# Kernel tuning notes

Measured on AMD Instinct MI355X. Metric: run time of the kernel, lower is better.

The kernel has to match this reference:

```python
import jax, jax.numpy as jnp
import numpy as np

C_CURV = 0.1            # curvature k
SC = float(np.sqrt(C_CURV))
EPS = 1e-7


def _mobius_add(x, y, c):
    x2 = jnp.sum(x * x, -1, keepdims=True)
    y2 = jnp.sum(y * y, -1, keepdims=True)
    xy = jnp.sum(x * y, -1, keepdims=True)
    num = (1 + 2 * c * xy + c * y2) * x + (1 - c * x2) * y
    den = 1 + 2 * c * xy + c * c * x2 * y2
    return num / jnp.maximum(den, 1e-12)


def _mobius_scalarmul(r, x, c):
    sc = jnp.sqrt(c)
    n = jnp.linalg.norm(x, axis=-1, keepdims=True)
    t = jnp.clip(sc * n, EPS, 1.0 - 1e-6)
    return jnp.tanh(r * jnp.arctanh(t)) * x / jnp.maximum(sc * n, EPS)


def setup_inputs() -> dict:
    key = jax.random.key(0)
    k0, k1, k2, k3, k4 = jax.random.split(key, 5)
    B, N, V, D, NC = 64, 1024, 50257, 128, 10
    token_ids = jax.random.randint(k0, (B, N), 0, V)
    mask = jax.random.randint(k1, (B, N), 0, 2).astype(bool)
    emb = (jax.random.normal(k2, (V, D), jnp.float32) * 0.02).at[0].set(0.0)  # pad_id=0 row zeroed
    Wo = jax.random.normal(k3, (D, D + 1), jnp.float32) / np.sqrt(D + 1)
    bo = jnp.zeros((D,), jnp.float32)
    Wf = jax.random.normal(k4, (NC, D), jnp.float32) / np.sqrt(D)
    bf = jnp.zeros((NC,), jnp.float32)
    return {"token_ids": token_ids, "mask": mask, "emb": emb, "Wo": Wo, "bo": bo, "Wf": Wf, "bf": bf}


def reference(token_ids, mask, emb, Wo, bo, Wf, bf):
    c, sc = C_CURV, SC
    D = emb.shape[1]
    # embedding lookup (tangent vectors at origin)
    v = emb[token_ids]                                            # (B,N,D)
    # Lorentz expmap0 -> hyperboloid points in D+1
    nv = jnp.maximum(jnp.linalg.norm(v, axis=-1, keepdims=True), EPS)
    x = jnp.concatenate([jnp.cosh(sc * nv) / sc,
                         jnp.sinh(sc * nv) * v / (sc * nv)], -1)  # (B,N,D+1)
    # single-head attention, scores = -<xi,xj>_L (Lorentz inner), masked softmax
    sgn = jnp.concatenate([-jnp.ones((1,)), jnp.ones((D,))]).astype(x.dtype)
    scores = -jnp.einsum('bid,bjd->bij', x * sgn, x) / np.sqrt(D + 1)
    scores = jnp.where(mask[:, None, :], scores, -1e9)
    w = jax.nn.softmax(scores, axis=-1)
    # riemannian value aggregation: Lorentz centroid (weighted sum renormalized to hyperboloid)
    mu = jnp.einsum('bij,bjd->bid', w, x)
    inner = jnp.einsum('bid,d,bid->bi', mu, sgn, mu)
    mu = mu / (sc * jnp.sqrt(jnp.maximum(-inner, EPS))[..., None])
    # output projection (D+1 -> D) then Poincare expmap0 so points lie in the ball
    u = jnp.einsum('bid,od->bio', mu, Wo) + bo                    # (B,N,D)
    nu = jnp.maximum(jnp.linalg.norm(u, axis=-1, keepdims=True), EPS)
    y = jnp.tanh(sc * nu) * u / (sc * nu)                         # (B,N,D) in ball
    # sequential masked Mobius pooling: left-fold mobius_add over valid tokens, then scalarmul 1/n
    def step(acc, xm):
        xi, mi = xm                                               # (B,D), (B,)
        new = _mobius_add(acc, xi, c)
        return jnp.where(mi[:, None], new, acc), None
    acc0 = jnp.zeros_like(y[:, 0, :])
    acc, _ = jax.lax.scan(step, acc0, (jnp.swapaxes(y, 0, 1), jnp.swapaxes(mask, 0, 1)))
    cnt = jnp.sum(mask, axis=1)
    r = (1.0 / jnp.maximum(cnt, 1))[:, None].astype(y.dtype)
    pooled = _mobius_scalarmul(r, acc, c)
    pooled = jnp.where((cnt > 0)[:, None], pooled, y[:, 0, :])    # empty rows fall back to first token
    # LorentzMLR head: logmap0 then linear
    npn = jnp.maximum(jnp.linalg.norm(pooled, axis=-1, keepdims=True), EPS)
    t = jnp.clip(sc * npn, EPS, 1.0 - 1e-6)
    vlog = jnp.arctanh(t) * pooled / (sc * npn)
    return vlog @ Wf.T + bf                                       # (B, num_classes)
```

## Files before the change

kernel.cpp:

```cpp
#include <hip/hip_runtime.h>
#include <math.h>

#define B_    64
#define N_    1024
#define D_    128
#define DP1   129
#define NC_   10
#define QB    128
#define KT    32
#define SCf   0.31622776601683794f
#define SCALE 0.08804509063256238f

typedef __bf16 bf16x8 __attribute__((ext_vector_type(8)));
typedef float  f32x16 __attribute__((ext_vector_type(16)));
typedef unsigned int  u32x4v __attribute__((ext_vector_type(4)));
typedef unsigned long long ull;

#define MFMA(a, b, c) __builtin_amdgcn_mfma_f32_32x32x16_bf16((a), (b), (c), 0, 0, 0)

static __device__ __forceinline__ unsigned pk_lo16(unsigned a, unsigned b) {
    return __builtin_amdgcn_perm(b, a, 0x05040100u);
}
static __device__ __forceinline__ unsigned pk_hi16(unsigned a, unsigned b) {
    return __builtin_amdgcn_perm(b, a, 0x07060302u);
}

static __device__ __forceinline__ float dpp_add_step(float f, int ctrl, int rmask) {
    if (ctrl == 0x111) { int t = __builtin_amdgcn_update_dpp(0, __builtin_bit_cast(int, f), 0x111, 0xf, 0xf, true); return f + __builtin_bit_cast(float, t); }
    if (ctrl == 0x112) { int t = __builtin_amdgcn_update_dpp(0, __builtin_bit_cast(int, f), 0x112, 0xf, 0xf, true); return f + __builtin_bit_cast(float, t); }
    if (ctrl == 0x114) { int t = __builtin_amdgcn_update_dpp(0, __builtin_bit_cast(int, f), 0x114, 0xf, 0xf, true); return f + __builtin_bit_cast(float, t); }
    if (ctrl == 0x118) { int t = __builtin_amdgcn_update_dpp(0, __builtin_bit_cast(int, f), 0x118, 0xf, 0xf, true); return f + __builtin_bit_cast(float, t); }
    if (ctrl == 0x142 && rmask == 0xa) { int t = __builtin_amdgcn_update_dpp(0, __builtin_bit_cast(int, f), 0x142, 0xa, 0xf, true); return f + __builtin_bit_cast(float, t); }
    { int t = __builtin_amdgcn_update_dpp(0, __builtin_bit_cast(int, f), 0x143, 0xc, 0xf, true); return f + __builtin_bit_cast(float, t); }
}

static __device__ __forceinline__ float wave_sum64(float f) {
    f = dpp_add_step(f, 0x111, 0xf);
    f = dpp_add_step(f, 0x112, 0xf);
    f = dpp_add_step(f, 0x114, 0xf);
    f = dpp_add_step(f, 0x118, 0xf);
    f = dpp_add_step(f, 0x142, 0xa);
    f = dpp_add_step(f, 0x143, 0xc);
    return __builtin_bit_cast(float, __builtin_amdgcn_readlane(__builtin_bit_cast(int, f), 63));
}

static __device__ __forceinline__ float half_sum32(float f, int half) {
    f = dpp_add_step(f, 0x111, 0xf);
    f = dpp_add_step(f, 0x112, 0xf);
    f = dpp_add_step(f, 0x114, 0xf);
    f = dpp_add_step(f, 0x118, 0xf);
    f = dpp_add_step(f, 0x142, 0xa);
    float s0 = __builtin_bit_cast(float, __builtin_amdgcn_readlane(__builtin_bit_cast(int, f), 31));
    float s1 = __builtin_bit_cast(float, __builtin_amdgcn_readlane(__builtin_bit_cast(int, f), 63));
    return half ? s1 : s0;
}

static __device__ __forceinline__ float readlane_f(float v, int lane) {
    return __builtin_bit_cast(float, __builtin_amdgcn_readlane(__builtin_bit_cast(int, v), lane));
}

static __device__ __forceinline__ bf16x8 ld_lds8(const __bf16* p) {
    union { bf16x8 v; ull q[2]; } u;
    u.q[0] = *(const ull*)(p);
    u.q[1] = *(const ull*)(p + 4);
    return u.v;
}

__global__ __launch_bounds__(256) void k_detect_mask(const int* __restrict__ mask_w,
                                                     int* __restrict__ flag) {
    __shared__ int bad;
    if (threadIdx.x == 0) bad = 0;
    __syncthreads();
    int local = 0;
    for (int i = threadIdx.x; i < 16384; i += 256) {
        int v = mask_w[i];
        if (v != 0 && v != 1) local = 1;
    }
    if (local) atomicOr(&bad, 1);
    __syncthreads();
    if (threadIdx.x == 0) *flag = bad;
}

static __device__ __forceinline__ int read_mask(const int* mw, int is_i8, int idx) {
    if (is_i8) return (int)((const unsigned char*)mw)[idx];
    return mw[idx];
}

__global__ __launch_bounds__(256) void k_prep_wo(const float* __restrict__ Wo,
                                                 __bf16* __restrict__ Woh,
                                                 __bf16* __restrict__ Wol) {
    int idx = blockIdx.x * 256 + threadIdx.x;
    if (idx >= 128 * 144) return;
    int o = idx / 144, d = idx - o * 144;
    float v = (d < DP1) ? Wo[o * DP1 + d] : 0.f;
    __bf16 h = (__bf16)v;
    Woh[idx] = h;
    Wol[idx] = (__bf16)(v - (float)h);
}

__global__ __launch_bounds__(256) void k_prep(const int* __restrict__ tok,
                                              const float* __restrict__ emb,
                                              __bf16* __restrict__ Xh, __bf16* __restrict__ Xl,
                                              float* __restrict__ X0g, float* __restrict__ X128g) {
    __shared__ float Xf[64][132];
    const int t = threadIdx.x, w = t >> 6, l = t & 63;
    const int base = blockIdx.x * 64;
    for (int it = 0; it < 16; ++it) {
        const int tk = w * 16 + it;
        const int id = tok[base + tk];
        const float2 v = ((const float2*)(emb + (size_t)id * D_))[l];
        float s = wave_sum64(v.x * v.x + v.y * v.y);
        float nv = fmaxf(sqrtf(s), 1e-7f);
        float a = SCf * nv;
        float a2 = a * a;
        float shc, ch;
        if (a < 0.5f) {
            shc = 1.f + a2 * (1.f/6.f) * (1.f + a2 * (1.f/20.f) * (1.f + a2 * (1.f/42.f)));
            ch  = 1.f + a2 * 0.5f * (1.f + a2 * (1.f/12.f) * (1.f + a2 * (1.f/30.f)));
        } else {
            float ea = __expf(a), ei = 1.f / ea;
            ch = 0.5f * (ea + ei);
            shc = 0.5f * (ea - ei) / a;
        }
        Xf[tk][1 + 2 * l] = v.x * shc;
        Xf[tk][2 + 2 * l] = v.y * shc;
        if (l == 0) Xf[tk][0] = ch / SCf;
    }
    __syncthreads();
    const int tk2 = t >> 2, dg = (t & 3) * 32;
    for (int i = 0; i < 32; i += 8) {
        bf16x8 hv, lv;
        #pragma unroll
        for (int j = 0; j < 8; ++j) {
            float f = Xf[tk2][dg + i + j];
            __bf16 h = (__bf16)f;
            hv[j] = h;
            lv[j] = (__bf16)(f - (float)h);
        }
        *(bf16x8*)(Xh + (size_t)(base + tk2) * D_ + dg + i) = hv;
        *(bf16x8*)(Xl + (size_t)(base + tk2) * D_ + dg + i) = lv;
    }
    if (t < 64) {
        X0g[base + t]   = Xf[t][0];
        X128g[base + t] = Xf[t][D_];
    }
}

__global__ __launch_bounds__(256, 2) void k_attn(
        const __bf16* __restrict__ Xh, const __bf16* __restrict__ Xl,
        const float* __restrict__ X0g, const float* __restrict__ X128g,
        const int* __restrict__ mask, const int* __restrict__ mflag,
        const __bf16* __restrict__ Woh, const __bf16* __restrict__ Wol,
        const float* __restrict__ bo,
        float* __restrict__ Y, float* __restrict__ Y2) {
    extern __shared__ char smem[];
    unsigned* KBI = (unsigned*)smem;
    unsigned* Pbi = (unsigned*)(smem + 33792);
    __shared__ float K0s[2][KT];
    __shared__ float K128s[2][KT];
    __shared__ int   Ms[2][KT];

    const int b    = blockIdx.x;
    const int qb   = blockIdx.y * QB;
    const int t    = threadIdx.x;
    const int w    = t >> 6;
    const int l    = t & 63;
    const int l31  = l & 31;
    const int half = l >> 5;
    const int is8  = *mflag;

    const size_t qrow = (size_t)(b * N_ + qb + w * 32 + l31);
    bf16x8 qfh[8], qfl[8];
    #pragma unroll
    for (int ks = 0; ks < 8; ++ks) {
        qfh[ks] = *(const bf16x8*)(Xh + qrow * D_ + ks * 16 + half * 8);
        qfl[ks] = *(const bf16x8*)(Xl + qrow * D_ + ks * 16 + half * 8);
    }
    float q0[16], q128[16];
    #pragma unroll
    for (int r = 0; r < 16; ++r) {
        const int qr = (r & 3) + 8 * (r >> 2) + 4 * half;
        q0[r]   = X0g[b * N_ + qb + w * 32 + qr];
        q128[r] = X128g[b * N_ + qb + w * 32 + qr];
    }

    const int skey = t >> 3, sck = t & 7;
    bf16x8 svh0, svh1, svl0, svl1;
    float  sK0 = 0.f, sK128 = 0.f;
    int    sM = 0;
    auto ldg_tile = [&](int kt) {
        const size_t kr = (size_t)(b * N_ + kt * KT + skey);
        svh0 = *(const bf16x8*)(Xh + kr * D_ + sck * 16);
        svh1 = *(const bf16x8*)(Xh + kr * D_ + sck * 16 + 8);
        svl0 = *(const bf16x8*)(Xl + kr * D_ + sck * 16);
        svl1 = *(const bf16x8*)(Xl + kr * D_ + sck * 16 + 8);
        if (t < KT) {
            sK0   = X0g[b * N_ + kt * KT + t];
            sK128 = X128g[b * N_ + kt * KT + t];
            sM    = read_mask(mask, is8, b * N_ + kt * KT + t);
        }
    };
    auto st_tile = [&](int buf) {
        unsigned* KI = KBI + buf * 4224;
        union { bf16x8 v; unsigned d[4]; } H0, H1, L0, L1;
        H0.v = svh0; H1.v = svh1; L0.v = svl0; L1.v = svl1;
        u32x4v o0 = { pk_lo16(H0.d[0], L0.d[0]), pk_hi16(H0.d[0], L0.d[0]),
                      pk_lo16(H0.d[1], L0.d[1]), pk_hi16(H0.d[1], L0.d[1]) };
        u32x4v o1 = { pk_lo16(H0.d[2], L0.d[2]), pk_hi16(H0.d[2], L0.d[2]),
                      pk_lo16(H0.d[3], L0.d[3]), pk_hi16(H0.d[3], L0.d[3]) };
        u32x4v o2 = { pk_lo16(H1.d[0], L1.d[0]), pk_hi16(H1.d[0], L1.d[0]),
                      pk_lo16(H1.d[1], L1.d[1]), pk_hi16(H1.d[1], L1.d[1]) };
        u32x4v o3 = { pk_lo16(H1.d[2], L1.d[2]), pk_hi16(H1.d[2], L1.d[2]),
                      pk_lo16(H1.d[3], L1.d[3]), pk_hi16(H1.d[3], L1.d[3]) };
        u32x4v* dst = (u32x4v*)(KI + skey * 132 + sck * 16);
        dst[0] = o0; dst[1] = o1; dst[2] = o2; dst[3] = o3;
        if (t < KT) { K0s[buf][t] = sK0; K128s[buf][t] = sK128; Ms[buf][t] = sM; }
    };

    f32x16 accM[4] = {};
    float  mu128p[16] = {};

    ldg_tile(0);
    st_tile(0);

    for (int kt = 0; kt < N_ / KT; ++kt) {
        __syncthreads();
        const int cur = kt & 1;
        const int ktn = (kt < 31) ? kt + 1 : 31;
        ldg_tile(ktn);

        const unsigned* KI = KBI + cur * 4224;

        f32x16 accS = {};
        #pragma unroll
        for (int ks = 0; ks < 8; ++ks) {
            const unsigned* p = KI + l31 * 132 + ks * 16 + half * 8;
            u32x4v ua = *(const u32x4v*)(p);
            u32x4v ub = *(const u32x4v*)(p + 4);
            union { bf16x8 v; unsigned d[4]; } BH, BL;
            BH.d[0] = pk_lo16(ua[0], ua[1]); BL.d[0] = pk_hi16(ua[0], ua[1]);
            BH.d[1] = pk_lo16(ua[2], ua[3]); BL.d[1] = pk_hi16(ua[2], ua[3]);
            BH.d[2] = pk_lo16(ub[0], ub[1]); BL.d[2] = pk_hi16(ub[0], ub[1]);
            BH.d[3] = pk_lo16(ub[2], ub[3]); BL.d[3] = pk_hi16(ub[2], ub[3]);
            accS = MFMA(qfh[ks], BH.v, accS);
            accS = MFMA(qfh[ks], BL.v, accS);
            accS = MFMA(qfl[ks], BH.v, accS);
        }
        const float k0v = K0s[cur][l31], k128v = K128s[cur][l31];
        const int   mv  = Ms[cur][l31];
        #pragma unroll
        for (int r = 0; r < 16; ++r) {
            float sc = (2.f * q0[r] * k0v - accS[r] - q128[r] * k128v) * SCALE;
            float e  = mv ? __expf(sc) : 0.f;
            mu128p[r] += e * k128v;
            __bf16 eh = (__bf16)e;
            __bf16 el = (__bf16)(e - (float)eh);
            unsigned pw = (unsigned)__builtin_bit_cast(unsigned short, eh)
                        | ((unsigned)__builtin_bit_cast(unsigned short, el) << 16);
            const int qr = (r & 3) + 8 * (r >> 2) + 4 * half;
            Pbi[w * 1152 + qr * 36 + l31] = pw;
        }

        #pragma unroll
        for (int ks = 0; ks < 2; ++ks) {
            const unsigned* pp = Pbi + w * 1152 + l31 * 36 + ks * 16 + half * 8;
            u32x4v pa = *(const u32x4v*)(pp);
            u32x4v pb = *(const u32x4v*)(pp + 4);
            union { bf16x8 v; unsigned d[4]; } AH, AL;
            AH.d[0] = pk_lo16(pa[0], pa[1]); AL.d[0] = pk_hi16(pa[0], pa[1]);
            AH.d[1] = pk_lo16(pa[2], pa[3]); AL.d[1] = pk_hi16(pa[2], pa[3]);
            AH.d[2] = pk_lo16(pb[0], pb[1]); AL.d[2] = pk_hi16(pb[0], pb[1]);
            AH.d[3] = pk_lo16(pb[2], pb[3]); AL.d[3] = pk_hi16(pb[2], pb[3]);
            #pragma unroll
            for (int nt = 0; nt < 4; ++nt) {
                const unsigned* kb = KI + (ks * 16 + half * 8) * 132 + nt * 32 + l31;
                unsigned u[8];
                #pragma unroll
                for (int j = 0; j < 8; ++j) u[j] = kb[j * 132];
                union { bf16x8 v; unsigned d[4]; } BH, BL;
                BH.d[0] = pk_lo16(u[0], u[1]); BL.d[0] = pk_hi16(u[0], u[1]);
                BH.d[1] = pk_lo16(u[2], u[3]); BL.d[1] = pk_hi16(u[2], u[3]);
                BH.d[2] = pk_lo16(u[4], u[5]); BL.d[2] = pk_hi16(u[4], u[5]);
                BH.d[3] = pk_lo16(u[6], u[7]); BL.d[3] = pk_hi16(u[6], u[7]);
                accM[nt] = MFMA(AH.v, BH.v, accM[nt]);
                accM[nt] = MFMA(AH.v, BL.v, accM[nt]);
                accM[nt] = MFMA(AL.v, BH.v, accM[nt]);
            }
        }

        st_tile(cur ^ 1);
    }

    #pragma unroll
    for (int r = 0; r < 16; ++r) mu128p[r] = half_sum32(mu128p[r], half);
    float rno[16];
    #pragma unroll
    for (int r = 0; r < 16; ++r) {
        float p = 0.f;
        #pragma unroll
        for (int nt = 0; nt < 4; ++nt) p += accM[nt][r] * accM[nt][r];
        if (l31 == 0) p -= 2.f * accM[0][r] * accM[0][r];
        p = half_sum32(p, half);
        float negI = -(p + mu128p[r] * mu128p[r]);
        negI = fmaxf(negI, 1e-7f);
        rno[r] = 1.f / (SCf * sqrtf(negI));
    }
    #pragma unroll
    for (int nt = 0; nt < 4; ++nt)
        #pragma unroll
        for (int r = 0; r < 16; ++r) accM[nt][r] *= rno[r];
    #pragma unroll
    for (int r = 0; r < 16; ++r) mu128p[r] *= rno[r];

    __syncthreads();
    __bf16* MuA = (__bf16*)smem + w * (32 * 148);
    #pragma unroll
    for (int r = 0; r < 16; ++r) {
        const int qr = (r & 3) + 8 * (r >> 2) + 4 * half;
        #pragma unroll
        for (int nt = 0; nt < 4; ++nt)
            MuA[qr * 148 + nt * 32 + l31] = (__bf16)accM[nt][r];
        if (l31 == 0) MuA[qr * 148 + 128] = (__bf16)mu128p[r];
        if (l31 >= 1 && l31 <= 15) MuA[qr * 148 + 128 + l31] = (__bf16)0.f;
    }
    bf16x8 Ah[9];
    #pragma unroll
    for (int ks = 0; ks < 9; ++ks) Ah[ks] = ld_lds8(MuA + l31 * 148 + ks * 16 + half * 8);
    #pragma unroll
    for (int r = 0; r < 16; ++r) {
        const int qr = (r & 3) + 8 * (r >> 2) + 4 * half;
        #pragma unroll
        for (int nt = 0; nt < 4; ++nt) {
            float m = accM[nt][r];
            MuA[qr * 148 + nt * 32 + l31] = (__bf16)(m - (float)(__bf16)m);
        }
        if (l31 == 0) {
            float m = mu128p[r];
            MuA[qr * 148 + 128] = (__bf16)(m - (float)(__bf16)m);
        }
    }
    bf16x8 Al[9];
    #pragma unroll
    for (int ks = 0; ks < 9; ++ks) Al[ks] = ld_lds8(MuA + l31 * 148 + ks * 16 + half * 8);

    f32x16 accU[4] = {};
    #pragma unroll
    for (int ks = 0; ks < 9; ++ks) {
        #pragma unroll
        for (int nt = 0; nt < 4; ++nt) {
            bf16x8 bh = *(const bf16x8*)(Woh + (size_t)(nt * 32 + l31) * 144 + ks * 16 + half * 8);
            bf16x8 bl = *(const bf16x8*)(Wol + (size_t)(nt * 32 + l31) * 144 + ks * 16 + half * 8);
            accU[nt] = MFMA(Ah[ks], bh, accU[nt]);
            accU[nt] = MFMA(Ah[ks], bl, accU[nt]);
            accU[nt] = MFMA(Al[ks], bh, accU[nt]);
        }
    }

    float bov[4];
    #pragma unroll
    for (int nt = 0; nt < 4; ++nt) bov[nt] = bo[nt * 32 + l31];
    #pragma unroll
    for (int r = 0; r < 16; ++r) {
        float p = 0.f;
        #pragma unroll
        for (int nt = 0; nt < 4; ++nt) {
            float uv = accU[nt][r] + bov[nt];
            accU[nt][r] = uv;
            p += uv * uv;
        }
        float nn = half_sum32(p, half);
        float nu = fmaxf(sqrtf(nn), 1e-7f);
        float aa = SCf * nu;
        float cf = tanhf(aa) / aa;
        const int qr = (r & 3) + 8 * (r >> 2) + 4 * half;
        const size_t row = (size_t)(b * N_ + qb + w * 32 + qr);
        #pragma unroll
        for (int nt = 0; nt < 4; ++nt)
            Y[row * D_ + nt * 32 + l31] = accU[nt][r] * cf;
        if (l31 == 0) Y2[row] = nn * cf * cf;
    }
}

__global__ __launch_bounds__(256) void k_gram(const float* __restrict__ Y,
                                              float* __restrict__ G) {
    const int c = blockIdx.x, b = blockIdx.y;
    const int t = threadIdx.x, w = t >> 6, l = t & 63;
    const int l31 = l & 31, half = l >> 5;
    const int rt = w >> 1, ct = w & 1;
    const size_t base = (size_t)(b * N_ + c * 64);
    const float* Ar = Y + (base + rt * 32 + l31) * D_;
    const float* Br = Y + (base + ct * 32 + l31) * D_;
    f32x16 acc = {};
    #pragma unroll
    for (int ks = 0; ks < 8; ++ks) {
        const int c0 = ks * 16 + half * 8;
        float4 a0 = *(const float4*)(Ar + c0);
        float4 a1 = *(const float4*)(Ar + c0 + 4);
        float4 b0 = *(const float4*)(Br + c0);
        float4 b1 = *(const float4*)(Br + c0 + 4);
        float av[8] = {a0.x, a0.y, a0.z, a0.w, a1.x, a1.y, a1.z, a1.w};
        float bv[8] = {b0.x, b0.y, b0.z, b0.w, b1.x, b1.y, b1.z, b1.w};
        bf16x8 ah, al, bh, bl;
        #pragma unroll
        for (int j = 0; j < 8; ++j) {
            __bf16 h = (__bf16)av[j]; ah[j] = h; al[j] = (__bf16)(av[j] - (float)h);
            __bf16 g = (__bf16)bv[j]; bh[j] = g; bl[j] = (__bf16)(bv[j] - (float)g);
        }
        acc = MFMA(ah, bh, acc);
        acc = MFMA(ah, bl, acc);
        acc = MFMA(al, bh, acc);
    }
    float* Gb = G + ((size_t)(b * 16 + c) << 12);
    #pragma unroll
    for (int r = 0; r < 16; ++r) {
        const int row = rt * 32 + (r & 3) + 8 * (r >> 2) + 4 * half;
        Gb[row * 64 + ct * 32 + l31] = acc[r];
    }
}

__global__ __launch_bounds__(64, 1) void k_pool(const float* __restrict__ Y,
                                                const float* __restrict__ Y2,
                                                const float* __restrict__ G,
                                                const int* __restrict__ mask,
                                                const int* __restrict__ mflag,
                                                const float* __restrict__ Wf,
                                                const float* __restrict__ bf_,
                                                float* __restrict__ out) {
    __shared__ float  prt[64][65];
    __shared__ double vb[D_];
    const int b = blockIdx.x, l = threadIdx.x;
    const int is8 = *mflag;

    int cl = 0;
    for (int i = l; i < N_; i += 64) cl += read_mask(mask, is8, b * N_ + i);
    const int cntT = (int)(wave_sum64((float)cl) + 0.5f);

    const float2* __restrict__ Yp = (const float2*)(Y + (size_t)b * N_ * D_) + l;
    const float*  __restrict__ Gp = G + ((size_t)b << 16) + l;
    const float*  __restrict__ Pp = Y2 + b * N_;

    float  GA[64], GB[64];
    float  py2A, py2B;
    int    msA, msB;
    float2 yring[2][16];

    #pragma unroll
    for (int i = 0; i < 64; ++i) GA[i] = Gp[i * 64];
    py2A = Pp[l];
    msA  = read_mask(mask, is8, b * N_ + l);
    #pragma unroll
    for (int k = 0; k < 16; ++k) yring[0][k] = Yp[(size_t)k * 64];

    float U0 = 0.f, U1 = 0.f, g = 0.f, Dh = 1.f, P = 0.f;

    auto chunk = [&](int c, float (&Gc)[64], float (&Gn)[64],
                     float py2c, float& py2n, int msc, int& msn) {
        const int cn = (c < 15) ? c + 1 : 15;
        #pragma unroll
        for (int i = 0; i < 64; ++i) Gn[i] = Gp[cn * 4096 + i * 64];
        py2n = Pp[cn * 64 + l];
        msn  = read_mask(mask, is8, b * N_ + cn * 64 + l);

        #pragma unroll
        for (int q = 0; q < 4; ++q) {
            #pragma unroll
            for (int k = 0; k < 16; ++k) {
                int gs = c * 64 + (q + 1) * 16 + k;
                if (gs > N_ - 1) gs = N_ - 1;
                yring[(q + 1) & 1][k] = Yp[(size_t)gs * 64];
            }
            #pragma unroll
            for (int k = 0; k < 16; ++k) {
                const int ir = q * 16 + k;
                const float2 yv  = yring[q & 1][k];
                const float  Gv  = Gc[ir];
                const float  py2 = readlane_f(py2c, ir);
                const bool   m   = (__builtin_amdgcn_readlane(msc, ir) != 0);
                const float Dsq   = Dh * Dh;
                const float Bh    = fmaf(-0.1f, P, Dsq);
                const float Donep = Dh * fmaf(0.1f, py2, 1.f);
                const float tP    = (0.01f * py2) * P;
                const float puy  = readlane_f(g, ir);
                const float Ahat = fmaf(0.2f, puy, Donep);
                float dh = fmaf(Dh, fmaf(0.2f, puy, Dh), tP);
                dh = fmaxf(dh, 1e-12f * Dsq);
                const float Draw = m ? dh : Dh;
                const float Am   = m ? Ahat : 1.f;
                const float Bm   = m ? Bh   : 0.f;
                const float Pn   = fmaf(Am, fmaf(Am, P, (2.f * Bm) * puy), (Bm * Bm) * py2);
                if ((k & 3) == 3) {
                    const int e = ilogbf(Draw);
                    const float Aef = ldexpf(Am, -e);
                    const float Bef = ldexpf(Bm, -e);
                    Dh = ldexpf(Draw, -e);
                    P  = ldexpf(Pn, -2 * e);
                    g  = fmaf(Aef, g, Bef * Gv);
                    U0 = fmaf(Aef, U0, Bef * yv.x);
                    U1 = fmaf(Aef, U1, Bef * yv.y);
                } else {
                    Dh = Draw;
                    P  = Pn;
                    g  = fmaf(Am, g, Bm * Gv);
                    U0 = fmaf(Am, U0, Bm * yv.x);
                    U1 = fmaf(Am, U1, Bm * yv.y);
                }
            }
        }
        if (c < 15) {
            const int nb = (c + 1) * 64;
            #pragma unroll
            for (int k0 = 0; k0 < 64; k0 += 16) {
                float2 tmp[16];
                #pragma unroll
                for (int k = 0; k < 16; ++k) tmp[k] = Yp[(size_t)(nb + k0 + k) * 64];
                #pragma unroll
                for (int k = 0; k < 16; ++k)
                    prt[k0 + k][l] = fmaf(U0, tmp[k].x, U1 * tmp[k].y);
            }
            float s0 = 0.f, s1 = 0.f, s2 = 0.f, s3 = 0.f;
            #pragma unroll
            for (int p = 0; p < 64; p += 4) {
                s0 += prt[l][p];     s1 += prt[l][p + 1];
                s2 += prt[l][p + 2]; s3 += prt[l][p + 3];
            }
            g = (s0 + s1) + (s2 + s3);
        }
    };

    for (int cc = 0; cc < 8; ++cc) {
        chunk(2 * cc,     GA, GB, py2A, py2B, msA, msB);
        chunk(2 * cc + 1, GB, GA, py2B, py2A, msB, msA);
    }

    const double SCd = 0.31622776601683794;
    const double sD = 1.0 / (double)Dh;
    double a0 = sD * (double)U0, a1 = sD * (double)U1;
    double n2 = fmax((double)P * (sD * sD), 0.0);
    double n = sqrt(n2);
    double tt = SCd * n;
    tt = fmin(fmax(tt, 1e-7), 1.0 - 1e-6);
    int cm = cntT > 0 ? cntT : 1;
    float rf = (float)(1.0 / (double)cm);
    double r = (double)rf;
    double dv = fmax(SCd * n, 1e-7);
    double f = tanh(r * atanh(tt)) / dv;
    double p0 = a0 * f, p1 = a1 * f;
    double q2;
    if (cntT == 0) {
        float2 y0v = *(const float2*)(Y + (size_t)(b * N_) * D_ + 2 * l);
        p0 = y0v.x; p1 = y0v.y;
        q2 = (double)Y2[b * N_];
    } else {
        q2 = f * f * n2;
    }
    double npn = fmax(sqrt(q2), 1e-7);
    double t2 = fmin(fmax(SCd * npn, 1e-7), 1.0 - 1e-6);
    double f2 = atanh(t2) / (SCd * npn);
    vb[2 * l]     = p0 * f2;
    vb[2 * l + 1] = p1 * f2;
    __syncthreads();

    if (l < NC_) {
        double o = (double)bf_[l];
        for (int d = 0; d < D_; ++d) o += vb[d] * (double)Wf[l * D_ + d];
        out[b * NC_ + l] = (float)o;
    }
}

extern "C" void kernel_launch(void* const* d_in, const int* in_sizes, int n_in,
                              void* d_out, int out_size, void* d_ws, size_t ws_size,
                              hipStream_t stream) {
    const int*   tok  = (const int*)d_in[0];
    const int*   mask = (const int*)d_in[1];
    const float* emb  = (const float*)d_in[2];
    const float* Wo   = (const float*)d_in[3];
    const float* bo   = (const float*)d_in[4];
    const float* Wf   = (const float*)d_in[5];
    const float* bf_  = (const float*)d_in[6];
    float* out = (float*)d_out;

    char* wsb = (char*)d_ws;
    __bf16* Xh   = (__bf16*)wsb;
    __bf16* Xl   = (__bf16*)(wsb + 16777216);
    float*  X0g  = (float*)(wsb + 33554432);
    float*  X128g= (float*)(wsb + 33816576);
    __bf16* Woh  = (__bf16*)(wsb + 34078720);
    __bf16* Wol  = (__bf16*)(wsb + 34115584);
    float*  Y    = (float*)(wsb + 34152448);
    float*  Y2   = (float*)(wsb + 67706880);
    int*    flag = (int*)(wsb + 67969024);
    float*  Gram = (float*)wsb;

    k_detect_mask<<<dim3(1), dim3(256), 0, stream>>>(mask, flag);
    k_prep_wo<<<dim3(72), dim3(256), 0, stream>>>(Wo, Woh, Wol);
    k_prep<<<dim3(B_ * N_ / 64), dim3(256), 0, stream>>>(tok, emb, Xh, Xl, X0g, X128g);
    k_attn<<<dim3(B_, N_ / QB), dim3(256), 52224, stream>>>(Xh, Xl, X0g, X128g, mask, flag,
                                                            Woh, Wol, bo, Y, Y2);
    k_gram<<<dim3(16, B_), dim3(256), 0, stream>>>(Y, Gram);
    k_pool<<<dim3(B_), dim3(64), 0, stream>>>(Y, Y2, Gram, mask, flag, Wf, bf_, out);
}
```

Before: 392.7 us.

## Fuse prep kernels into one launch and compute Gram blocks inside attention

Merges mask detection, Wo split and embedding prep into a single kernel launch, using extra blocks for the small side tasks. When the workspace is large enough, the attention kernel stages its output Y tile in shared memory and computes the 64x64 Gram blocks directly with split-bf16 MFMAs. This removes the separate k_gram pass that re-reads Y from global memory and saves launch overhead. In exchange it adds extra syncs and LDS reuse at the tail of attention, and requires an extra 16MB workspace region, falling back to the old path otherwise.

New measurement: 388.0 us. Within noise of the previous version (-1.2%).

```diff
diff --git a/kernel.cpp b/kernel.cpp
--- a/kernel.cpp
+++ b/kernel.cpp
@@ -66,44 +66,46 @@
     return u.v;
 }
 
-__global__ __launch_bounds__(256) void k_detect_mask(const int* __restrict__ mask_w,
-                                                     int* __restrict__ flag) {
-    __shared__ int bad;
-    if (threadIdx.x == 0) bad = 0;
-    __syncthreads();
-    int local = 0;
-    for (int i = threadIdx.x; i < 16384; i += 256) {
-        int v = mask_w[i];
-        if (v != 0 && v != 1) local = 1;
-    }
-    if (local) atomicOr(&bad, 1);
-    __syncthreads();
-    if (threadIdx.x == 0) *flag = bad;
-}
-
 static __device__ __forceinline__ int read_mask(const int* mw, int is_i8, int idx) {
     if (is_i8) return (int)((const unsigned char*)mw)[idx];
     return mw[idx];
 }
 
-__global__ __launch_bounds__(256) void k_prep_wo(const float* __restrict__ Wo,
-                                                 __bf16* __restrict__ Woh,
-                                                 __bf16* __restrict__ Wol) {
-    int idx = blockIdx.x * 256 + threadIdx.x;
-    if (idx >= 128 * 144) return;
-    int o = idx / 144, d = idx - o * 144;
-    float v = (d < DP1) ? Wo[o * DP1 + d] : 0.f;
-    __bf16 h = (__bf16)v;
-    Woh[idx] = h;
-    Wol[idx] = (__bf16)(v - (float)h);
-}
-
-__global__ __launch_bounds__(256) void k_prep(const int* __restrict__ tok,
-                                              const float* __restrict__ emb,
-                                              __bf16* __restrict__ Xh, __bf16* __restrict__ Xl,
-                                              float* __restrict__ X0g, float* __restrict__ X128g) {
+__global__ __launch_bounds__(256) void k_pre(const int* __restrict__ tok,
+                                             const float* __restrict__ emb,
+                                             __bf16* __restrict__ Xh, __bf16* __restrict__ Xl,
+                                             float* __restrict__ X0g, float* __restrict__ X128g,
+                                             const int* __restrict__ mask_w, int* __restrict__ flag,
+                                             const float* __restrict__ Wo,
+                                             __bf16* __restrict__ Woh, __bf16* __restrict__ Wol) {
+    const int t = threadIdx.x;
+    if (blockIdx.x >= 1024) {
+        if (blockIdx.x == 1096) {
+            __shared__ int bad;
+            if (t == 0) bad = 0;
+            __syncthreads();
+            int local = 0;
+            for (int i = t; i < 16384; i += 256) {
+                int v = mask_w[i];
+                if (v != 0 && v != 1) local = 1;
+            }
+            if (local) atomicOr(&bad, 1);
+            __syncthreads();
+            if (t == 0) *flag = bad;
+        } else {
+            int idx = (blockIdx.x - 1024) * 256 + t;
+            if (idx < 128 * 144) {
+                int o = idx / 144, d = idx - o * 144;
+                float v = (d < DP1) ? Wo[o * DP1 + d] : 0.f;
+                __bf16 h = (__bf16)v;
+                Woh[idx] = h;
+                Wol[idx] = (__bf16)(v - (float)h);
+            }
+        }
+        return;
+    }
     __shared__ float Xf[64][132];
-    const int t = threadIdx.x, w = t >> 6, l = t & 63;
+    const int w = t >> 6, l = t & 63;
     const int base = blockIdx.x * 64;
     for (int it = 0; it < 16; ++it) {
         const int tk = w * 16 + it;
@@ -146,13 +148,15 @@
     }
 }
 
+template<int FG>
 __global__ __launch_bounds__(256, 2) void k_attn(
         const __bf16* __restrict__ Xh, const __bf16* __restrict__ Xl,
         const float* __restrict__ X0g, const float* __restrict__ X128g,
         const int* __restrict__ mask, const int* __restrict__ mflag,
         const __bf16* __restrict__ Woh, const __bf16* __restrict__ Wol,
         const float* __restrict__ bo,
-        float* __restrict__ Y, float* __restrict__ Y2) {
+        float* __restrict__ Y, float* __restrict__ Y2,
+        float* __restrict__ G) {
     extern __shared__ char smem[];
     unsigned* KBI = (unsigned*)smem;
     unsigned* Pbi = (unsigned*)(smem + 33792);
@@ -375,9 +379,60 @@
         const int qr = (r & 3) + 8 * (r >> 2) + 4 * half;
         const size_t row = (size_t)(b * N_ + qb + w * 32 + qr);
         #pragma unroll
-        for (int nt = 0; nt < 4; ++nt)
-            Y[row * D_ + nt * 32 + l31] = accU[nt][r] * cf;
+        for (int nt = 0; nt < 4; ++nt) {
+            float yv = accU[nt][r] * cf;
+            accU[nt][r] = yv;
+            Y[row * D_ + nt * 32 + l31] = yv;
+        }
         if (l31 == 0) Y2[row] = nn * cf * cf;
+    }
+
+    if (FG) {
+        float* Yt = (float*)smem;
+        const int rt = w >> 1, ct = w & 1;
+        #pragma unroll
+        for (int ph = 0; ph < 2; ++ph) {
+            __syncthreads();
+            if ((w >> 1) == ph) {
+                const int rloc = (w & 1) * 32;
+                #pragma unroll
+                for (int r = 0; r < 16; ++r) {
+                    const int qr = (r & 3) + 8 * (r >> 2) + 4 * half;
+                    #pragma unroll
+                    for (int nt = 0; nt < 4; ++nt)
+                        Yt[(rloc + qr) * 132 + nt * 32 + l31] = accU[nt][r];
+                }
+            }
+            __syncthreads();
+            f32x16 gacc = {};
+            #pragma unroll
+            for (int ks = 0; ks < 8; ++ks) {
+                const int c0 = ks * 16 + half * 8;
+                const float* Ar = Yt + (rt * 32 + l31) * 132 + c0;
+                const float* Br = Yt + (ct * 32 + l31) * 132 + c0;
+                float4 a0 = *(const float4*)(Ar);
+                float4 a1 = *(const float4*)(Ar + 4);
+                float4 b0 = *(const float4*)(Br);
+                float4 b1 = *(const float4*)(Br + 4);
+                float av[8] = {a0.x, a0.y, a0.z, a0.w, a1.x, a1.y, a1.z, a1.w};
+                float bv[8] = {b0.x, b0.y, b0.z, b0.w, b1.x, b1.y, b1.z, b1.w};
+                bf16x8 ah, al, bh, bl;
+                #pragma unroll
+                for (int j = 0; j < 8; ++j) {
+                    __bf16 h = (__bf16)av[j]; ah[j] = h; al[j] = (__bf16)(av[j] - (float)h);
+                    __bf16 g2 = (__bf16)bv[j]; bh[j] = g2; bl[j] = (__bf16)(bv[j] - (float)g2);
+                }
+                gacc = MFMA(ah, bh, gacc);
+                gacc = MFMA(ah, bl, gacc);
+                gacc = MFMA(al, bh, gacc);
+            }
+            float* Gb = G + ((size_t)(b * 16 + 2 * blockIdx.y + ph) << 12);
+            #pragma unroll
+            for (int r = 0; r < 16; ++r) {
+                const int row = rt * 32 + (r & 3) + 8 * (r >> 2) + 4 * half;
+                Gb[row * 64 + ct * 32 + l31] = gacc[r];
+            }
+        }
     }
 }
 
@@ -589,13 +644,21 @@
     float*  Y    = (float*)(wsb + 34152448);
     float*  Y2   = (float*)(wsb + 67706880);
     int*    flag = (int*)(wsb + 67969024);
-    float*  Gram = (float*)wsb;
-
-    k_detect_mask<<<dim3(1), dim3(256), 0, stream>>>(mask, flag);
-    k_prep_wo<<<dim3(72), dim3(256), 0, stream>>>(Wo, Woh, Wol);
-    k_prep<<<dim3(B_ * N_ / 64), dim3(256), 0, stream>>>(tok, emb, Xh, Xl, X0g, X128g);
-    k_attn<<<dim3(B_, N_ / QB), dim3(256), 52224, stream>>>(Xh, Xl, X0g, X128g, mask, flag,
-                                                            Woh, Wol, bo, Y, Y2);
-    k_gram<<<dim3(16, B_), dim3(256), 0, stream>>>(Y, Gram);
-    k_pool<<<dim3(B_), dim3(64), 0, stream>>>(Y, Y2, Gram, mask, flag, Wf, bf_, out);
-}
+    float*  GramA= (float*)wsb;
+    float*  GramF= (float*)(wsb + 67973120);
+
+    const bool fg = ws_size >= 67973120ull + 16777216ull;
+
+    k_pre<<<dim3(1097), dim3(256), 0, stream>>>(tok, emb, Xh, Xl, X0g, X128g,
+                                                mask, flag, Wo, Woh, Wol);
+    if (fg) {
+        k_attn<1><<<dim3(B_, N_ / QB), dim3(256), 52224, stream>>>(Xh, Xl, X0g, X128g, mask, flag,
+                                                                   Woh, Wol, bo, Y, Y2, GramF);
+        k_pool<<<dim3(B_), dim3(64), 0, stream>>>(Y, Y2, GramF, mask, flag, Wf, bf_, out);
+    } else {
+        k_attn<0><<<dim3(B_, N_ / QB), dim3(256), 52224, stream>>>(Xh, Xl, X0g, X128g, mask, flag,
+                                                                   Woh, Wol, bo, Y, Y2, GramA);
+        k_gram<<<dim3(16, B_), dim3(256), 0, stream>>>(Y, GramA);
+        k_pool<<<dim3(B_), dim3(64), 0, stream>>>(Y, Y2, GramA, mask, flag, Wf, bf_, out);
+    }
+}
```
